# Performance work log

Hardware: AMD Instinct MI355X
Metric: run time of the kernel (lower is better)

The kernel has to match this reference:

```python
import jax, jax.numpy as jnp
import numpy as np

K = 10  # value-iteration steps


def _conv(x, w):
    # NCHW x OIHW -> NCHW, stride 1, SAME padding (pad=2 for 5x5, pad=0 for 1x1)
    return jax.lax.conv_general_dilated(
        x, w, window_strides=(1, 1), padding='SAME',
        dimension_numbers=('NCHW', 'OIHW', 'NCHW'))


def setup_inputs() -> dict:
    key = jax.random.key(0)
    ks = jax.random.split(key, 6)
    B, H, W = 64, 64, 64
    dim_h, n_hat, n_act = 150, 8, 4
    maze = jax.random.randint(ks[0], (B, H, W), 0, 3)
    # fixed embedding table from the torch module
    emb = jnp.array([[0.0, 0.0], [1.0, 0.0], [0.0, 10.0]], dtype=jnp.float32)
    encode_w = jax.random.normal(ks[1], (dim_h, 2, 5, 5), dtype=jnp.float32) * 0.05
    encode_b = jnp.zeros((dim_h,), dtype=jnp.float32)
    r_w = jax.random.normal(ks[2], (1, dim_h, 1, 1), dtype=jnp.float32) * 0.05
    q_w = jax.random.normal(ks[3], (n_hat, 1, 5, 5), dtype=jnp.float32) * 0.05
    # torch inits self.w to zeros; use small randn so the recurrence is non-trivial
    w = jax.random.normal(ks[4], (n_hat, 1, 5, 5), dtype=jnp.float32) * 0.05
    fc_w = jax.random.normal(ks[5], (n_act, n_hat), dtype=jnp.float32) * 0.1
    return dict(maze=maze, emb=emb, encode_w=encode_w, encode_b=encode_b,
                r_w=r_w, q_w=q_w, w=w, fc_w=fc_w)


def reference(maze, emb, encode_w, encode_b, r_w, q_w, w, fc_w):
    # embed: [B,H,W] -> [B,H,W,2] -> [B,2,H,W]
    m = emb[maze].transpose(0, 3, 1, 2)
    h = _conv(m, encode_w) + encode_b[None, :, None, None]  # [B,150,H,W]
    r = _conv(h, r_w)                                        # [B,1,H,W]
    q = _conv(r, q_w)                                        # [B,8,H,W]
    wk = jnp.concatenate([q_w, w], axis=1)                   # [8,2,5,5]

    def step(q, _):
        v = jnp.max(q, axis=1, keepdims=True)                # [B,1,H,W]
        q = _conv(jnp.concatenate([r, v], axis=1), wk)       # [B,8,H,W]
        return q, None

    q, _ = jax.lax.scan(step, q, None, length=K)
    q = q.transpose(0, 2, 3, 1)                              # [B,H,W,8]
    return q @ fc_w.T                                        # [B,H,W,4]
```

## Files before the change

### kernel.cpp

```cpp
#include <hip/hip_runtime.h>
#include <hip/hip_bf16.h>


#define NHAT 8
#define DIMH 150

typedef float v2f __attribute__((ext_vector_type(2)));

__global__ __launch_bounds__(512) void rq_kernel(
    const int* __restrict__ maze, const float* __restrict__ emb,
    const float* __restrict__ encode_w, const float* __restrict__ encode_b,
    const float* __restrict__ r_w, const float* __restrict__ q_w,
    float* __restrict__ q0g) {
  __shared__ float wpart[5][50];
  __shared__ float bpart[152];
  __shared__ float weff[2][25];
  __shared__ float Ts[4][25];
  __shared__ float bsh;
  __shared__ v2f qw2[25][4];
  __shared__ unsigned char mzt[24][68];
  __shared__ float rt[20][68];

  int tid = threadIdx.x;
  int b = blockIdx.y, A0 = blockIdx.x * 16;

  if (tid < 100) {
    int k = tid >> 2, j = tid & 3;
    qw2[k][j] = (v2f){q_w[(2 * j) * 25 + k], q_w[(2 * j + 1) * 25 + k]};
  }
  if (tid >= 256 && tid < 506) {
    int t2 = tid - 256;
    int chunk = t2 / 50, ik = t2 % 50;
    int i = ik / 25, k = ik % 25;
    int c0 = chunk * 30;
    float s = 0.f;
    for (int c = c0; c < c0 + 30; ++c)
      s += r_w[c] * encode_w[c * 50 + i * 25 + k];
    wpart[chunk][ik] = s;
  }
  if (tid >= 100 && tid < 250) {
    int c = tid - 100;
    bpart[c] = r_w[c] * encode_b[c];
  }
  for (int i = tid; i < 24 * 68; i += 512) {
    int mr = i / 68, mc = i % 68;
    int gy = A0 - 4 + mr, gx = mc - 2;
    unsigned char v = 3;
    if (gy >= 0 && gy < 64 && gx >= 0 && gx < 64)
      v = (unsigned char)maze[(b * 64 + gy) * 64 + gx];
    mzt[mr][mc] = v;
  }
  __syncthreads();
  if (tid < 50) {
    float s = 0.f;
#pragma unroll
    for (int ch = 0; ch < 5; ++ch) s += wpart[ch][tid];
    weff[tid / 25][tid % 25] = s;
  }
  if (tid == 50) {
    float s = 0.f;
    for (int c = 0; c < 150; ++c) s += bpart[c];
    bsh = s;
  }
  __syncthreads();
  if (tid < 100) {
    int val = tid / 25, k = tid % 25;
    float t = 0.f;
    if (val < 3) t = weff[0][k] * emb[val * 2] + weff[1][k] * emb[val * 2 + 1];
    Ts[val][k] = t;
  }
  __syncthreads();
  for (int i = tid; i < 20 * 68; i += 512) {
    int rr = i / 68, cc = i % 68;
    int gy = A0 - 2 + rr, gx = cc - 2;
    float v = 0.f;
    if (gy >= 0 && gy < 64 && gx >= 0 && gx < 64) {
      v = bsh;
#pragma unroll
      for (int ky = 0; ky < 5; ++ky)
#pragma unroll
        for (int kx = 0; kx < 5; ++kx)
          v += Ts[mzt[rr + ky][cc - 2 + kx]][ky * 5 + kx];
    }
    rt[rr][cc] = v;
  }
  __syncthreads();
  for (int i = tid; i < 16 * 64; i += 512) {
    int ly = i >> 6, gx = i & 63;
    int gy = A0 + ly;
    v2f acc[4];
#pragma unroll
    for (int j = 0; j < 4; ++j) acc[j] = (v2f){0.f, 0.f};
#pragma unroll
    for (int ky = 0; ky < 5; ++ky)
#pragma unroll
      for (int kx = 0; kx < 5; ++kx) {
        int k = ky * 5 + kx;
        float vv = rt[ly + ky][gx + kx];
        v2f vv2 = (v2f){vv, vv};
#pragma unroll
        for (int j = 0; j < 4; ++j) acc[j] += qw2[k][j] * vv2;
      }
    size_t base = ((size_t)(b * 64 + gy) * 2) * 64 + gx;
    *(float4*)&q0g[(base)*4] = make_float4(acc[0].x, acc[0].y, acc[1].x, acc[1].y);
    *(float4*)&q0g[(base + 64) * 4] =
        make_float4(acc[2].x, acc[2].y, acc[3].x, acc[3].y);
  }
}

__global__ __launch_bounds__(512, 2) void vi_kernel(
    const float* __restrict__ q0g, const float* __restrict__ w,
    const float* __restrict__ fc_w, float* __restrict__ out) {
  __shared__ __align__(16) float vbuf[2][60][68];
  __shared__ __align__(16) float tmp[52][2][64];
  __shared__ v2f wl2[25][4];

  int tid = threadIdx.x;
  int b = blockIdx.y, a0 = blockIdx.x * 16;
  int wave = tid >> 6, lane = tid & 63;
  int half = wave & 1, slot = wave >> 1;
  int roff = lane >> 4, i4 = (lane & 15) * 4;

  if (tid < 100) {
    int k = tid >> 2, j = tid & 3;
    wl2[k][j] = (v2f){w[(2 * j) * 25 + k], w[(2 * j + 1) * 25 + k]};
  }
  for (int i = tid; i < 2 * 60 * 68; i += 512) ((float*)vbuf)[i] = 0.f;
  __syncthreads();

  v2f wr0[25], wr1[25];
#pragma unroll
  for (int k = 0; k < 25; ++k) {
    wr0[k] = wl2[k][2 * half];
    wr1[k] = wl2[k][2 * half + 1];
  }

  const float* q0b = q0g + (size_t)b * 64 * 2 * 64 * 4;
  int cur = 0;

  {
    int s = max(0, a0 - 20), e = min(64, a0 + 36);
    int gx = lane;
    for (int r = s + wave; r < e; r += 8) {
      float4 f0 = *(const float4*)&q0b[(((size_t)r * 2 + 0) * 64 + gx) * 4];
      float4 f1 = *(const float4*)&q0b[(((size_t)r * 2 + 1) * 64 + gx) * 4];
      float m = fmaxf(fmaxf(fmaxf(f0.x, f0.y), fmaxf(f0.z, f0.w)),
                      fmaxf(fmaxf(f1.x, f1.y), fmaxf(f1.z, f1.w)));
      vbuf[0][r - a0 + 22][gx + 2] = m;
    }
  }
  __syncthreads();

  for (int t = 1; t <= 9; ++t) {
    int hh = 2 * (10 - t);
    int s = max(0, a0 - hh), e = min(64, a0 + 16 + hh);
    for (int rb = s + 4 * slot; rb < e; rb += 16) {
      int r = rb + roff;
      if (r < e) {
        int lr = r - a0 + 22;
        const float4* qp =
            (const float4*)&q0b[(((size_t)r * 2 + half) * 64 + i4) * 4];
        float4 qv0 = qp[0], qv1 = qp[1], qv2 = qp[2], qv3 = qp[3];
        v2f aA[4], aB[4];
        aA[0] = (v2f){qv0.x, qv0.y}; aB[0] = (v2f){qv0.z, qv0.w};
        aA[1] = (v2f){qv1.x, qv1.y}; aB[1] = (v2f){qv1.z, qv1.w};
        aA[2] = (v2f){qv2.x, qv2.y}; aB[2] = (v2f){qv2.z, qv2.w};
        aA[3] = (v2f){qv3.x, qv3.y}; aB[3] = (v2f){qv3.z, qv3.w};
#pragma unroll
        for (int jj = 0; jj < 5; ++jj) {
          const float* row = &vbuf[cur][lr - 2 + jj][i4];
          float4 fa = *(const float4*)row;
          float4 fb = *(const float4*)(row + 4);
          float f[8] = {fa.x, fa.y, fa.z, fa.w, fb.x, fb.y, fb.z, fb.w};
#pragma unroll
          for (int kx = 0; kx < 5; ++kx) {
            int k = jj * 5 + kx;
            v2f w0 = wr0[k], w1 = wr1[k];
#pragma unroll
            for (int j = 0; j < 4; ++j) {
              v2f vv2 = (v2f){f[j + kx], f[j + kx]};
              aA[j] += w0 * vv2;
              aB[j] += w1 * vv2;
            }
          }
        }
        float m0 = fmaxf(fmaxf(aA[0].x, aA[0].y), fmaxf(aB[0].x, aB[0].y));
        float m1 = fmaxf(fmaxf(aA[1].x, aA[1].y), fmaxf(aB[1].x, aB[1].y));
        float m2 = fmaxf(fmaxf(aA[2].x, aA[2].y), fmaxf(aB[2].x, aB[2].y));
        float m3 = fmaxf(fmaxf(aA[3].x, aA[3].y), fmaxf(aB[3].x, aB[3].y));
        *(float4*)&tmp[lr - 4][half][i4] = make_float4(m0, m1, m2, m3);
      }
    }
    __syncthreads();
    int n = e - s;
    for (int idx = tid; idx < n * 64; idx += 512) {
      int rr = idx >> 6, px = idx & 63;
      int lr2 = s - a0 + 22 + rr;
      vbuf[cur ^ 1][lr2][px + 2] =
          fmaxf(tmp[lr2 - 4][0][px], tmp[lr2 - 4][1][px]);
    }
    __syncthreads();
    cur ^= 1;
  }

  float fcp[4][4];
#pragma unroll
  for (int a = 0; a < 4; ++a)
#pragma unroll
    for (int cc = 0; cc < 4; ++cc) fcp[a][cc] = fc_w[a * 8 + 4 * half + cc];
  float* ptmp = (float*)tmp;

  {
    int r = a0 + 4 * slot + roff;
    int lr = r - a0 + 22;
    const float4* qp =
        (const float4*)&q0b[(((size_t)r * 2 + half) * 64 + i4) * 4];
    float4 qv0 = qp[0], qv1 = qp[1], qv2 = qp[2], qv3 = qp[3];
    v2f aA[4], aB[4];
    aA[0] = (v2f){qv0.x, qv0.y}; aB[0] = (v2f){qv0.z, qv0.w};
    aA[1] = (v2f){qv1.x, qv1.y}; aB[1] = (v2f){qv1.z, qv1.w};
    aA[2] = (v2f){qv2.x, qv2.y}; aB[2] = (v2f){qv2.z, qv2.w};
    aA[3] = (v2f){qv3.x, qv3.y}; aB[3] = (v2f){qv3.z, qv3.w};
#pragma unroll
    for (int jj = 0; jj < 5; ++jj) {
      const float* row = &vbuf[cur][lr - 2 + jj][i4];
      float4 fa = *(const float4*)row;
      float4 fb = *(const float4*)(row + 4);
      float f[8] = {fa.x, fa.y, fa.z, fa.w, fb.x, fb.y, fb.z, fb.w};
#pragma unroll
      for (int kx = 0; kx < 5; ++kx) {
        int k = jj * 5 + kx;
        v2f w0 = wr0[k], w1 = wr1[k];
#pragma unroll
        for (int j = 0; j < 4; ++j) {
          v2f vv2 = (v2f){f[j + kx], f[j + kx]};
          aA[j] += w0 * vv2;
          aB[j] += w1 * vv2;
        }
      }
    }
    float4 pp[4];
#pragma unroll
    for (int j = 0; j < 4; ++j) {
      float q0v = aA[j].x, q1v = aA[j].y, q2v = aB[j].x, q3v = aB[j].y;
      pp[j].x = fcp[0][0] * q0v + fcp[0][1] * q1v + fcp[0][2] * q2v + fcp[0][3] * q3v;
      pp[j].y = fcp[1][0] * q0v + fcp[1][1] * q1v + fcp[1][2] * q2v + fcp[1][3] * q3v;
      pp[j].z = fcp[2][0] * q0v + fcp[2][1] * q1v + fcp[2][2] * q2v + fcp[2][3] * q3v;
      pp[j].w = fcp[3][0] * q0v + fcp[3][1] * q1v + fcp[3][2] * q2v + fcp[3][3] * q3v;
    }
    if (half == 1) {
#pragma unroll
      for (int j = 0; j < 4; ++j)
        *(float4*)&ptmp[(((r - a0) * 64) + i4 + j) * 4] = pp[j];
    }
    __syncthreads();
    if (half == 0) {
#pragma unroll
      for (int j = 0; j < 4; ++j) {
        float4 o = *(const float4*)&ptmp[(((r - a0) * 64) + i4 + j) * 4];
        o.x += pp[j].x; o.y += pp[j].y; o.z += pp[j].z; o.w += pp[j].w;
        *(float4*)&out[((size_t)((b * 64 + r) * 64 + i4 + j)) * 4] = o;
      }
    }
  }
}

extern "C" void kernel_launch(void* const* d_in, const int* in_sizes, int n_in,
                              void* d_out, int out_size, void* d_ws, size_t ws_size,
                              hipStream_t stream) {
  const int* maze = (const int*)d_in[0];
  const float* emb = (const float*)d_in[1];
  const float* encode_w = (const float*)d_in[2];
  const float* encode_b = (const float*)d_in[3];
  const float* r_w = (const float*)d_in[4];
  const float* q_w = (const float*)d_in[5];
  const float* w = (const float*)d_in[6];
  const float* fc_w = (const float*)d_in[7];
  float* out = (float*)d_out;

  float* q0g = (float*)d_ws;

  rq_kernel<<<dim3(4, 64), 512, 0, stream>>>(maze, emb, encode_w, encode_b,
                                             r_w, q_w, q0g);
  vi_kernel<<<dim3(4, 64), 512, 0, stream>>>(q0g, w, fc_w, out);
}
```

Before: 114.2 us.

## Merge channel halves within a wave via shuffles, drop tmp buffer and barrier

The two channel halves of each pixel move into one wavefront (lanes 0-31 and 32-63), so the max over channels and the fc reduction become __shfl_xor exchanges instead of going through a shared tmp buffer. This removes one __syncthreads and an extra LDS pass per value-iteration step, and frees the tmp shared array, which may help occupancy. As a second change, the q0 loads now sit ahead of the conv loop and are added after it, giving the loads time to land. The new lane-to-pixel mapping changes the LDS access pattern and adds shuffle work.

```diff
diff --git a/kernel.cpp b/kernel.cpp
--- a/kernel.cpp
+++ b/kernel.cpp
@@ -112,14 +112,15 @@
     const float* __restrict__ q0g, const float* __restrict__ w,
     const float* __restrict__ fc_w, float* __restrict__ out) {
   __shared__ __align__(16) float vbuf[2][60][68];
-  __shared__ __align__(16) float tmp[52][2][64];
   __shared__ v2f wl2[25][4];
 
   int tid = threadIdx.x;
   int b = blockIdx.y, a0 = blockIdx.x * 16;
   int wave = tid >> 6, lane = tid & 63;
-  int half = wave & 1, slot = wave >> 1;
-  int roff = lane >> 4, i4 = (lane & 15) * 4;
+  int chh = lane >> 5;
+  int l5 = lane & 31;
+  int roff = l5 >> 4;
+  int i4 = (l5 & 15) * 4;
 
   if (tid < 100) {
     int k = tid >> 2, j = tid & 3;
@@ -131,8 +132,8 @@
   v2f wr0[25], wr1[25];
 #pragma unroll
   for (int k = 0; k < 25; ++k) {
-    wr0[k] = wl2[k][2 * half];
-    wr1[k] = wl2[k][2 * half + 1];
+    wr0[k] = wl2[k][2 * chh];
+    wr1[k] = wl2[k][2 * chh + 1];
   }
 
   const float* q0b = q0g + (size_t)b * 64 * 2 * 64 * 4;
@@ -154,18 +155,19 @@
   for (int t = 1; t <= 9; ++t) {
     int hh = 2 * (10 - t);
     int s = max(0, a0 - hh), e = min(64, a0 + 16 + hh);
-    for (int rb = s + 4 * slot; rb < e; rb += 16) {
+    for (int rb = s + 2 * wave; rb < e; rb += 16) {
       int r = rb + roff;
       if (r < e) {
         int lr = r - a0 + 22;
         const float4* qp =
-            (const float4*)&q0b[(((size_t)r * 2 + half) * 64 + i4) * 4];
+            (const float4*)&q0b[(((size_t)r * 2 + chh) * 64 + i4) * 4];
         float4 qv0 = qp[0], qv1 = qp[1], qv2 = qp[2], qv3 = qp[3];
         v2f aA[4], aB[4];
-        aA[0] = (v2f){qv0.x, qv0.y}; aB[0] = (v2f){qv0.z, qv0.w};
-        aA[1] = (v2f){qv1.x, qv1.y}; aB[1] = (v2f){qv1.z, qv1.w};
-        aA[2] = (v2f){qv2.x, qv2.y}; aB[2] = (v2f){qv2.z, qv2.w};
-        aA[3] = (v2f){qv3.x, qv3.y}; aB[3] = (v2f){qv3.z, qv3.w};
+#pragma unroll
+        for (int j = 0; j < 4; ++j) {
+          aA[j] = (v2f){0.f, 0.f};
+          aB[j] = (v2f){0.f, 0.f};
+        }
 #pragma unroll
         for (int jj = 0; jj < 5; ++jj) {
           const float* row = &vbuf[cur][lr - 2 + jj][i4];
@@ -184,20 +186,23 @@
             }
           }
         }
+        aA[0] += (v2f){qv0.x, qv0.y}; aB[0] += (v2f){qv0.z, qv0.w};
+        aA[1] += (v2f){qv1.x, qv1.y}; aB[1] += (v2f){qv1.z, qv1.w};
+        aA[2] += (v2f){qv2.x, qv2.y}; aB[2] += (v2f){qv2.z, qv2.w};
+        aA[3] += (v2f){qv3.x, qv3.y}; aB[3] += (v2f){qv3.z, qv3.w};
         float m0 = fmaxf(fmaxf(aA[0].x, aA[0].y), fmaxf(aB[0].x, aB[0].y));
         float m1 = fmaxf(fmaxf(aA[1].x, aA[1].y), fmaxf(aB[1].x, aB[1].y));
         float m2 = fmaxf(fmaxf(aA[2].x, aA[2].y), fmaxf(aB[2].x, aB[2].y));
         float m3 = fmaxf(fmaxf(aA[3].x, aA[3].y), fmaxf(aB[3].x, aB[3].y));
-        *(float4*)&tmp[lr - 4][half][i4] = make_float4(m0, m1, m2, m3);
+        float n0 = fmaxf(m0, __shfl_xor(m0, 32));
+        float n1 = fmaxf(m1, __shfl_xor(m1, 32));
+        float n2 = fmaxf(m2, __shfl_xor(m2, 32));
+        float n3 = fmaxf(m3, __shfl_xor(m3, 32));
+        if (chh == 0)
+          *(v2f*)&vbuf[cur ^ 1][lr][i4 + 2] = (v2f){n0, n1};
+        else
+          *(v2f*)&vbuf[cur ^ 1][lr][i4 + 4] = (v2f){n2, n3};
       }
-    }
-    __syncthreads();
-    int n = e - s;
-    for (int idx = tid; idx < n * 64; idx += 512) {
-      int rr = idx >> 6, px = idx & 63;
-      int lr2 = s - a0 + 22 + rr;
-      vbuf[cur ^ 1][lr2][px + 2] =
-          fmaxf(tmp[lr2 - 4][0][px], tmp[lr2 - 4][1][px]);
     }
     __syncthreads();
     cur ^= 1;
@@ -207,20 +212,20 @@
 #pragma unroll
   for (int a = 0; a < 4; ++a)
 #pragma unroll
-    for (int cc = 0; cc < 4; ++cc) fcp[a][cc] = fc_w[a * 8 + 4 * half + cc];
-  float* ptmp = (float*)tmp;
+    for (int cc = 0; cc < 4; ++cc) fcp[a][cc] = fc_w[a * 8 + 4 * chh + cc];
 
   {
-    int r = a0 + 4 * slot + roff;
+    int r = a0 + 2 * wave + roff;
     int lr = r - a0 + 22;
     const float4* qp =
-        (const float4*)&q0b[(((size_t)r * 2 + half) * 64 + i4) * 4];
+        (const float4*)&q0b[(((size_t)r * 2 + chh) * 64 + i4) * 4];
     float4 qv0 = qp[0], qv1 = qp[1], qv2 = qp[2], qv3 = qp[3];
     v2f aA[4], aB[4];
-    aA[0] = (v2f){qv0.x, qv0.y}; aB[0] = (v2f){qv0.z, qv0.w};
-    aA[1] = (v2f){qv1.x, qv1.y}; aB[1] = (v2f){qv1.z, qv1.w};
-    aA[2] = (v2f){qv2.x, qv2.y}; aB[2] = (v2f){qv2.z, qv2.w};
-    aA[3] = (v2f){qv3.x, qv3.y}; aB[3] = (v2f){qv3.z, qv3.w};
+#pragma unroll
+    for (int j = 0; j < 4; ++j) {
+      aA[j] = (v2f){0.f, 0.f};
+      aB[j] = (v2f){0.f, 0.f};
+    }
 #pragma unroll
     for (int jj = 0; jj < 5; ++jj) {
       const float* row = &vbuf[cur][lr - 2 + jj][i4];
@@ -239,6 +244,10 @@
         }
       }
     }
+    aA[0] += (v2f){qv0.x, qv0.y}; aB[0] += (v2f){qv0.z, qv0.w};
+    aA[1] += (v2f){qv1.x, qv1.y}; aB[1] += (v2f){qv1.z, qv1.w};
+    aA[2] += (v2f){qv2.x, qv2.y}; aB[2] += (v2f){qv2.z, qv2.w};
+    aA[3] += (v2f){qv3.x, qv3.y}; aB[3] += (v2f){qv3.z, qv3.w};
     float4 pp[4];
 #pragma unroll
     for (int j = 0; j < 4; ++j) {
@@ -248,19 +257,17 @@
       pp[j].z = fcp[2][0] * q0v + fcp[2][1] * q1v + fcp[2][2] * q2v + fcp[2][3] * q3v;
       pp[j].w = fcp[3][0] * q0v + fcp[3][1] * q1v + fcp[3][2] * q2v + fcp[3][3] * q3v;
     }
-    if (half == 1) {
+#pragma unroll
+    for (int j = 0; j < 4; ++j) {
+      pp[j].x += __shfl_xor(pp[j].x, 32);
+      pp[j].y += __shfl_xor(pp[j].y, 32);
+      pp[j].z += __shfl_xor(pp[j].z, 32);
+      pp[j].w += __shfl_xor(pp[j].w, 32);
+    }
+    if (chh == 0) {
 #pragma unroll
       for (int j = 0; j < 4; ++j)
-        *(float4*)&ptmp[(((r - a0) * 64) + i4 + j) * 4] = pp[j];
-    }
-    __syncthreads();
-    if (half == 0) {
-#pragma unroll
-      for (int j = 0; j < 4; ++j) {
-        float4 o = *(const float4*)&ptmp[(((r - a0) * 64) + i4 + j) * 4];
-        o.x += pp[j].x; o.y += pp[j].y; o.z += pp[j].z; o.w += pp[j].w;
-        *(float4*)&out[((size_t)((b * 64 + r) * 64 + i4 + j)) * 4] = o;
-      }
+        *(float4*)&out[((size_t)((b * 64 + r) * 64 + i4 + j)) * 4] = pp[j];
     }
   }
 }
```

After: 109.3 us. -4.3%, faster.

## Split VI channels across lane quarters with shuffle max, drop tmp pass

Applied to the files above, without the earlier changes.

Rewrites the value-iteration kernel so each lane handles one channel pair for 8 pixels, and the four channel pairs sit in lane quarters of the same wave. The channel max is taken with cross-lane shuffles and written straight into the next value buffer. This removes the shared tmp buffer, one barrier and a reduction pass per step. The q0 workspace layout changes to [row][chanpair][x][2] to match, and the block grows to 1024 threads. The cost is more shuffles, fewer registers per thread, and a final fc stage that uses only half the waves.

```diff
diff --git a/kernel.cpp b/kernel.cpp
--- a/kernel.cpp
+++ b/kernel.cpp
@@ -101,51 +101,49 @@
 #pragma unroll
         for (int j = 0; j < 4; ++j) acc[j] += qw2[k][j] * vv2;
       }
-    size_t base = ((size_t)(b * 64 + gy) * 2) * 64 + gx;
-    *(float4*)&q0g[(base)*4] = make_float4(acc[0].x, acc[0].y, acc[1].x, acc[1].y);
-    *(float4*)&q0g[(base + 64) * 4] =
-        make_float4(acc[2].x, acc[2].y, acc[3].x, acc[3].y);
+#pragma unroll
+    for (int j = 0; j < 4; ++j)
+      *(v2f*)&q0g[(((size_t)(b * 64 + gy) * 4 + j) * 64 + gx) * 2] = acc[j];
   }
 }
 
-__global__ __launch_bounds__(512, 2) void vi_kernel(
+__global__ __launch_bounds__(1024, 4) void vi_kernel(
     const float* __restrict__ q0g, const float* __restrict__ w,
     const float* __restrict__ fc_w, float* __restrict__ out) {
   __shared__ __align__(16) float vbuf[2][60][68];
-  __shared__ __align__(16) float tmp[52][2][64];
   __shared__ v2f wl2[25][4];
 
   int tid = threadIdx.x;
   int b = blockIdx.y, a0 = blockIdx.x * 16;
   int wave = tid >> 6, lane = tid & 63;
-  int half = wave & 1, slot = wave >> 1;
-  int roff = lane >> 4, i4 = (lane & 15) * 4;
+  int cq = lane >> 4;
+  int roff = (lane >> 3) & 1;
+  int p8 = (lane & 7) * 8;
 
   if (tid < 100) {
     int k = tid >> 2, j = tid & 3;
     wl2[k][j] = (v2f){w[(2 * j) * 25 + k], w[(2 * j + 1) * 25 + k]};
   }
-  for (int i = tid; i < 2 * 60 * 68; i += 512) ((float*)vbuf)[i] = 0.f;
-  __syncthreads();
-
-  v2f wr0[25], wr1[25];
-#pragma unroll
-  for (int k = 0; k < 25; ++k) {
-    wr0[k] = wl2[k][2 * half];
-    wr1[k] = wl2[k][2 * half + 1];
-  }
-
-  const float* q0b = q0g + (size_t)b * 64 * 2 * 64 * 4;
+  for (int i = tid; i < 2 * 60 * 68; i += 1024) ((float*)vbuf)[i] = 0.f;
+  __syncthreads();
+
+  v2f wr[25];
+#pragma unroll
+  for (int k = 0; k < 25; ++k) wr[k] = wl2[k][cq];
+
+  const float* q0b = q0g + (size_t)b * 64 * 4 * 64 * 2;
   int cur = 0;
 
   {
     int s = max(0, a0 - 20), e = min(64, a0 + 36);
     int gx = lane;
-    for (int r = s + wave; r < e; r += 8) {
-      float4 f0 = *(const float4*)&q0b[(((size_t)r * 2 + 0) * 64 + gx) * 4];
-      float4 f1 = *(const float4*)&q0b[(((size_t)r * 2 + 1) * 64 + gx) * 4];
-      float m = fmaxf(fmaxf(fmaxf(f0.x, f0.y), fmaxf(f0.z, f0.w)),
-                      fmaxf(fmaxf(f1.x, f1.y), fmaxf(f1.z, f1.w)));
+    for (int r = s + wave; r < e; r += 16) {
+      v2f a0v = *(const v2f*)&q0b[(((size_t)r * 4 + 0) * 64 + gx) * 2];
+      v2f a1v = *(const v2f*)&q0b[(((size_t)r * 4 + 1) * 64 + gx) * 2];
+      v2f a2v = *(const v2f*)&q0b[(((size_t)r * 4 + 2) * 64 + gx) * 2];
+      v2f a3v = *(const v2f*)&q0b[(((size_t)r * 4 + 3) * 64 + gx) * 2];
+      float m = fmaxf(fmaxf(fmaxf(a0v.x, a0v.y), fmaxf(a1v.x, a1v.y)),
+                      fmaxf(fmaxf(a2v.x, a2v.y), fmaxf(a3v.x, a3v.y)));
       vbuf[0][r - a0 + 22][gx + 2] = m;
     }
   }
@@ -154,113 +152,109 @@
   for (int t = 1; t <= 9; ++t) {
     int hh = 2 * (10 - t);
     int s = max(0, a0 - hh), e = min(64, a0 + 16 + hh);
-    for (int rb = s + 4 * slot; rb < e; rb += 16) {
+    for (int rb = s + 2 * wave; rb < e; rb += 32) {
       int r = rb + roff;
       if (r < e) {
         int lr = r - a0 + 22;
         const float4* qp =
-            (const float4*)&q0b[(((size_t)r * 2 + half) * 64 + i4) * 4];
+            (const float4*)&q0b[(((size_t)r * 4 + cq) * 64 + p8) * 2];
         float4 qv0 = qp[0], qv1 = qp[1], qv2 = qp[2], qv3 = qp[3];
-        v2f aA[4], aB[4];
-        aA[0] = (v2f){qv0.x, qv0.y}; aB[0] = (v2f){qv0.z, qv0.w};
-        aA[1] = (v2f){qv1.x, qv1.y}; aB[1] = (v2f){qv1.z, qv1.w};
-        aA[2] = (v2f){qv2.x, qv2.y}; aB[2] = (v2f){qv2.z, qv2.w};
-        aA[3] = (v2f){qv3.x, qv3.y}; aB[3] = (v2f){qv3.z, qv3.w};
+        v2f aA[8];
+#pragma unroll
+        for (int j = 0; j < 8; ++j) aA[j] = (v2f){0.f, 0.f};
 #pragma unroll
         for (int jj = 0; jj < 5; ++jj) {
-          const float* row = &vbuf[cur][lr - 2 + jj][i4];
+          const float* row = &vbuf[cur][lr - 2 + jj][p8];
           float4 fa = *(const float4*)row;
           float4 fb = *(const float4*)(row + 4);
-          float f[8] = {fa.x, fa.y, fa.z, fa.w, fb.x, fb.y, fb.z, fb.w};
+          float4 fc = *(const float4*)(row + 8);
+          float f[12] = {fa.x, fa.y, fa.z, fa.w, fb.x, fb.y,
+                         fb.z, fb.w, fc.x, fc.y, fc.z, fc.w};
 #pragma unroll
           for (int kx = 0; kx < 5; ++kx) {
-            int k = jj * 5 + kx;
-            v2f w0 = wr0[k], w1 = wr1[k];
-#pragma unroll
-            for (int j = 0; j < 4; ++j) {
+            v2f wk = wr[jj * 5 + kx];
+#pragma unroll
+            for (int j = 0; j < 8; ++j) {
               v2f vv2 = (v2f){f[j + kx], f[j + kx]};
-              aA[j] += w0 * vv2;
-              aB[j] += w1 * vv2;
+              aA[j] += wk * vv2;
             }
           }
         }
-        float m0 = fmaxf(fmaxf(aA[0].x, aA[0].y), fmaxf(aB[0].x, aB[0].y));
-        float m1 = fmaxf(fmaxf(aA[1].x, aA[1].y), fmaxf(aB[1].x, aB[1].y));
-        float m2 = fmaxf(fmaxf(aA[2].x, aA[2].y), fmaxf(aB[2].x, aB[2].y));
-        float m3 = fmaxf(fmaxf(aA[3].x, aA[3].y), fmaxf(aB[3].x, aB[3].y));
-        *(float4*)&tmp[lr - 4][half][i4] = make_float4(m0, m1, m2, m3);
+        aA[0] += (v2f){qv0.x, qv0.y}; aA[1] += (v2f){qv0.z, qv0.w};
+        aA[2] += (v2f){qv1.x, qv1.y}; aA[3] += (v2f){qv1.z, qv1.w};
+        aA[4] += (v2f){qv2.x, qv2.y}; aA[5] += (v2f){qv2.z, qv2.w};
+        aA[6] += (v2f){qv3.x, qv3.y}; aA[7] += (v2f){qv3.z, qv3.w};
+        float m0 = fmaxf(aA[0].x, aA[0].y), m1 = fmaxf(aA[1].x, aA[1].y);
+        float m2 = fmaxf(aA[2].x, aA[2].y), m3 = fmaxf(aA[3].x, aA[3].y);
+        float m4 = fmaxf(aA[4].x, aA[4].y), m5 = fmaxf(aA[5].x, aA[5].y);
+        float m6 = fmaxf(aA[6].x, aA[6].y), m7 = fmaxf(aA[7].x, aA[7].y);
+        m0 = fmaxf(m0, __shfl_xor(m0, 16)); m0 = fmaxf(m0, __shfl_xor(m0, 32));
+        m1 = fmaxf(m1, __shfl_xor(m1, 16)); m1 = fmaxf(m1, __shfl_xor(m1, 32));
+        m2 = fmaxf(m2, __shfl_xor(m2, 16)); m2 = fmaxf(m2, __shfl_xor(m2, 32));
+        m3 = fmaxf(m3, __shfl_xor(m3, 16)); m3 = fmaxf(m3, __shfl_xor(m3, 32));
+        m4 = fmaxf(m4, __shfl_xor(m4, 16)); m4 = fmaxf(m4, __shfl_xor(m4, 32));
+        m5 = fmaxf(m5, __shfl_xor(m5, 16)); m5 = fmaxf(m5, __shfl_xor(m5, 32));
+        m6 = fmaxf(m6, __shfl_xor(m6, 16)); m6 = fmaxf(m6, __shfl_xor(m6, 32));
+        m7 = fmaxf(m7, __shfl_xor(m7, 16)); m7 = fmaxf(m7, __shfl_xor(m7, 32));
+        if (cq == 0) {
+          *(v2f*)&vbuf[cur ^ 1][lr][2 + p8] = (v2f){m0, m1};
+          *(float4*)&vbuf[cur ^ 1][lr][4 + p8] = make_float4(m2, m3, m4, m5);
+          *(v2f*)&vbuf[cur ^ 1][lr][8 + p8] = (v2f){m6, m7};
+        }
       }
-    }
-    __syncthreads();
-    int n = e - s;
-    for (int idx = tid; idx < n * 64; idx += 512) {
-      int rr = idx >> 6, px = idx & 63;
-      int lr2 = s - a0 + 22 + rr;
-      vbuf[cur ^ 1][lr2][px + 2] =
-          fmaxf(tmp[lr2 - 4][0][px], tmp[lr2 - 4][1][px]);
     }
     __syncthreads();
     cur ^= 1;
   }
 
-  float fcp[4][4];
-#pragma unroll
-  for (int a = 0; a < 4; ++a)
-#pragma unroll
-    for (int cc = 0; cc < 4; ++cc) fcp[a][cc] = fc_w[a * 8 + 4 * half + cc];
-  float* ptmp = (float*)tmp;
-
-  {
-    int r = a0 + 4 * slot + roff;
+  if (wave < 8) {
+    int r = a0 + 2 * wave + roff;
     int lr = r - a0 + 22;
     const float4* qp =
-        (const float4*)&q0b[(((size_t)r * 2 + half) * 64 + i4) * 4];
+        (const float4*)&q0b[(((size_t)r * 4 + cq) * 64 + p8) * 2];
     float4 qv0 = qp[0], qv1 = qp[1], qv2 = qp[2], qv3 = qp[3];
-    v2f aA[4], aB[4];
-    aA[0] = (v2f){qv0.x, qv0.y}; aB[0] = (v2f){qv0.z, qv0.w};
-    aA[1] = (v2f){qv1.x, qv1.y}; aB[1] = (v2f){qv1.z, qv1.w};
-    aA[2] = (v2f){qv2.x, qv2.y}; aB[2] = (v2f){qv2.z, qv2.w};
-    aA[3] = (v2f){qv3.x, qv3.y}; aB[3] = (v2f){qv3.z, qv3.w};
+    v2f aA[8];
+#pragma unroll
+    for (int j = 0; j < 8; ++j) aA[j] = (v2f){0.f, 0.f};
 #pragma unroll
     for (int jj = 0; jj < 5; ++jj) {
-      const float* row = &vbuf[cur][lr - 2 + jj][i4];
+      const float* row = &vbuf[cur][lr - 2 + jj][p8];
       float4 fa = *(const float4*)row;
       float4 fb = *(const float4*)(row + 4);
-      float f[8] = {fa.x, fa.y, fa.z, fa.w, fb.x, fb.y, fb.z, fb.w};
+      float4 fc = *(const float4*)(row + 8);
+      float f[12] = {fa.x, fa.y, fa.z, fa.w, fb.x, fb.y,
+                     fb.z, fb.w, fc.x, fc.y, fc.z, fc.w};
 #pragma unroll
       for (int kx = 0; kx < 5; ++kx) {
-        int k = jj * 5 + kx;
-        v2f w0 = wr0[k], w1 = wr1[k];
-#pragma unroll
-        for (int j = 0; j < 4; ++j) {
+        v2f wk = wr[jj * 5 + kx];
+#pragma unroll
+        for (int j = 0; j < 8; ++j) {
           v2f vv2 = (v2f){f[j + kx], f[j + kx]};
-          aA[j] += w0 * vv2;
-          aB[j] += w1 * vv2;
+          aA[j] += wk * vv2;
         }
       }
     }
-    float4 pp[4];
-#pragma unroll
-    for (int j = 0; j < 4; ++j) {
-      float q0v = aA[j].x, q1v = aA[j].y, q2v = aB[j].x, q3v = aB[j].y;
-      pp[j].x = fcp[0][0] * q0v + fcp[0][1] * q1v + fcp[0][2] * q2v + fcp[0][3] * q3v;
-      pp[j].y = fcp[1][0] * q0v + fcp[1][1] * q1v + fcp[1][2] * q2v + fcp[1][3] * q3v;
-      pp[j].z = fcp[2][0] * q0v + fcp[2][1] * q1v + fcp[2][2] * q2v + fcp[2][3] * q3v;
-      pp[j].w = fcp[3][0] * q0v + fcp[3][1] * q1v + fcp[3][2] * q2v + fcp[3][3] * q3v;
-    }
-    if (half == 1) {
-#pragma unroll
-      for (int j = 0; j < 4; ++j)
-        *(float4*)&ptmp[(((r - a0) * 64) + i4 + j) * 4] = pp[j];
-    }
-    __syncthreads();
-    if (half == 0) {
-#pragma unroll
-      for (int j = 0; j < 4; ++j) {
-        float4 o = *(const float4*)&ptmp[(((r - a0) * 64) + i4 + j) * 4];
-        o.x += pp[j].x; o.y += pp[j].y; o.z += pp[j].z; o.w += pp[j].w;
-        *(float4*)&out[((size_t)((b * 64 + r) * 64 + i4 + j)) * 4] = o;
-      }
+    aA[0] += (v2f){qv0.x, qv0.y}; aA[1] += (v2f){qv0.z, qv0.w};
+    aA[2] += (v2f){qv1.x, qv1.y}; aA[3] += (v2f){qv1.z, qv1.w};
+    aA[4] += (v2f){qv2.x, qv2.y}; aA[5] += (v2f){qv2.z, qv2.w};
+    aA[6] += (v2f){qv3.x, qv3.y}; aA[7] += (v2f){qv3.z, qv3.w};
+    v2f fcp2[4];
+#pragma unroll
+    for (int a = 0; a < 4; ++a)
+      fcp2[a] = (v2f){fc_w[a * 8 + 2 * cq], fc_w[a * 8 + 2 * cq + 1]};
+#pragma unroll
+    for (int j = 0; j < 8; ++j) {
+      float p0 = fcp2[0].x * aA[j].x + fcp2[0].y * aA[j].y;
+      float p1 = fcp2[1].x * aA[j].x + fcp2[1].y * aA[j].y;
+      float p2 = fcp2[2].x * aA[j].x + fcp2[2].y * aA[j].y;
+      float p3 = fcp2[3].x * aA[j].x + fcp2[3].y * aA[j].y;
+      p0 += __shfl_xor(p0, 16); p0 += __shfl_xor(p0, 32);
+      p1 += __shfl_xor(p1, 16); p1 += __shfl_xor(p1, 32);
+      p2 += __shfl_xor(p2, 16); p2 += __shfl_xor(p2, 32);
+      p3 += __shfl_xor(p3, 16); p3 += __shfl_xor(p3, 32);
+      if (cq == 0)
+        *(float4*)&out[((size_t)((b * 64 + r) * 64 + p8 + j)) * 4] =
+            make_float4(p0, p1, p2, p3);
     }
   }
 }
@@ -282,5 +276,5 @@
 
   rq_kernel<<<dim3(4, 64), 512, 0, stream>>>(maze, emb, encode_w, encode_b,
                                              r_w, q_w, q0g);
-  vi_kernel<<<dim3(4, 64), 512, 0, stream>>>(q0g, w, fc_w, out);
+  vi_kernel<<<dim3(4, 64), 1024, 0, stream>>>(q0g, w, fc_w, out);
 }
```

New measurement: 124.8 us. 9.3% more time.
